# Optimization experiments

Hardware: AMD Instinct MI355X
Metric: run time of the kernel (lower is better)

Reference implementation:

```python
import jax, jax.numpy as jnp
import numpy as np

NUM_TAGS = 128
NUM_FEATURES = 500000
B, T, F = 64, 512, 8


def setup_inputs() -> dict:
    key = jax.random.key(0)
    ks = jax.random.split(key, 6)
    feats = jax.random.randint(ks[0], (B, T, F), 0, NUM_FEATURES)
    tags = jax.random.randint(ks[1], (B, T), 0, NUM_TAGS)
    # original init: uniform(-0.01, 0.01)
    state_weights = jax.random.uniform(ks[2], (NUM_TAGS, NUM_FEATURES), minval=-0.01, maxval=0.01, dtype=jnp.float32)
    transitions = jax.random.uniform(ks[3], (NUM_TAGS, NUM_TAGS), minval=-0.01, maxval=0.01, dtype=jnp.float32)
    start_transitions = jax.random.uniform(ks[4], (NUM_TAGS,), minval=-0.01, maxval=0.01, dtype=jnp.float32)
    end_transitions = jax.random.uniform(ks[5], (NUM_TAGS,), minval=-0.01, maxval=0.01, dtype=jnp.float32)
    return dict(feats=feats, tags=tags, state_weights=state_weights,
                transitions=transitions, start_transitions=start_transitions,
                end_transitions=end_transitions)


def reference(feats, tags, state_weights, transitions, start_transitions, end_transitions):
    """Batched CRF negative log-likelihood per sentence: logZ - gold_score. Returns [B]."""
    # emissions[b,t,k] = sum_f state_weights[k, feats[b,t,f]]  (emissions_for_sentence)
    emissions = jnp.take(state_weights, feats, axis=1).sum(-1)   # [K,B,T]
    emissions = jnp.moveaxis(emissions, 0, -1)                    # [B,T,K]

    # log_partition: forward algorithm over T via scan
    alpha0 = start_transitions[None, :] + emissions[:, 0]         # [B,K]

    def step(alpha, em_t):
        # scores[b,i,j] = alpha[b,i] + transitions[i,j]
        scores = alpha[:, :, None] + transitions[None, :, :]
        return jax.nn.logsumexp(scores, axis=1) + em_t, None

    em_rest = jnp.moveaxis(emissions[:, 1:], 1, 0)                # [T-1,B,K]
    alphaT, _ = jax.lax.scan(step, alpha0, em_rest)
    log_z = jax.nn.logsumexp(alphaT + end_transitions[None, :], axis=1)   # [B]

    # gold_score, vectorized over batch
    em_gold = jnp.take_along_axis(emissions, tags[..., None], axis=2)[..., 0].sum(axis=1)  # [B]
    trans_gold = transitions[tags[:, :-1], tags[:, 1:]].sum(axis=1)                        # [B]
    gold = start_transitions[tags[:, 0]] + end_transitions[tags[:, -1]] + em_gold + trans_gold

    return log_z - gold
```

## Files before the change

### kernel.cpp

```cpp
#include <hip/hip_runtime.h>

#define NUM_TAGS 128
#define NUM_FEATS 500000
#define BB 64
#define TT 512
#define FF 8

#define SWT_BYTES 256000000ull
#define EM_BYTES  16777216ull
#define NEED_FULL (SWT_BYTES + EM_BYTES)

typedef float f2 __attribute__((ext_vector_type(2)));

#define AP(j) ((((j) >> 5) * 36) + ((j) & 31))

__device__ __forceinline__ void barrier_lds() {
  asm volatile("s_waitcnt lgkmcnt(0)" ::: "memory");
  __builtin_amdgcn_s_barrier();
  __builtin_amdgcn_sched_barrier(0);
}

__device__ __forceinline__ float quad_sum_dpp(float r) {
  int t1 = __builtin_amdgcn_mov_dpp(__builtin_bit_cast(int, r), 0xB1, 0xF, 0xF, true);
  r += __builtin_bit_cast(float, t1);
  int t2 = __builtin_amdgcn_mov_dpp(__builtin_bit_cast(int, r), 0x4E, 0xF, 0xF, true);
  r += __builtin_bit_cast(float, t2);
  return r;
}

__global__ __launch_bounds__(256) void transpose_kernel(
    const float* __restrict__ sw, float* __restrict__ swT) {
  __shared__ float tile[32][129];
  const int f0 = blockIdx.x * 32;
  const int t = threadIdx.x;
  const int fi = t & 31, kb = t >> 5;
#pragma unroll
  for (int it = 0; it < 16; ++it) {
    int k = kb + it * 8;
    tile[fi][k] = sw[(size_t)k * NUM_FEATS + f0 + fi];
  }
  __syncthreads();
  const int k2 = t & 127, fo = t >> 7;
#pragma unroll
  for (int it = 0; it < 16; ++it) {
    int f2i = fo + it * 2;
    swT[(size_t)(f0 + f2i) * NUM_TAGS + k2] = tile[f2i][k2];
  }
}

__global__ __launch_bounds__(128) void gather_t_kernel(
    const int* __restrict__ feats, const float* __restrict__ swT,
    float* __restrict__ em_exp) {
  const int token = blockIdx.x;
  const int k = threadIdx.x;
  const int* f = feats + token * FF;
  float s = 0.f;
#pragma unroll
  for (int i = 0; i < FF; ++i) s += swT[(size_t)f[i] * NUM_TAGS + k];
  em_exp[(size_t)token * NUM_TAGS + k] = __expf(s);
}

__global__ __launch_bounds__(128) void gather_f_kernel(
    const int* __restrict__ feats, const float* __restrict__ sw,
    float* __restrict__ em_exp) {
  const int token = blockIdx.x;
  const int k = threadIdx.x;
  const int* f = feats + token * FF;
  const float* row = sw + (size_t)k * NUM_FEATS;
  float s = 0.f;
#pragma unroll
  for (int i = 0; i < FF; ++i) s += row[f[i]];
  em_exp[(size_t)token * NUM_TAGS + k] = __expf(s);
}

#define EINIT(I) (f2){__expf(trans[(32 * q + 2 * (I)) * NUM_TAGS + j]), \
                      __expf(trans[(32 * q + 2 * (I) + 1) * NUM_TAGS + j])}

#define STEP(EV, T, SRC, DST) do {                                          \
  float ev_ = (EV);                                                         \
  int tp_ = (T) + 4; if (tp_ > TT - 1) tp_ = TT - 1;                        \
  (EV) = embx[tp_ * NUM_TAGS + j];                    \
  const float4* a4_ = (const float4*)((SRC) + q * 36);                      \
  float4 A0 = a4_[0], A1 = a4_[1], A2 = a4_[2], A3 = a4_[3];                \
  float4 A4 = a4_[4], A5 = a4_[5], A6 = a4_[6], A7 = a4_[7];                \
  f2 ac0 = {0.f, 0.f}, ac1 = {0.f, 0.f};                                    \
  ac0 += (f2){A0.x, A0.y} * e00;  ac1 += (f2){A0.z, A0.w} * e01;            \
  ac0 += (f2){A1.x, A1.y} * e02;  ac1 += (f2){A1.z, A1.w} * e03;            \
  ac0 += (f2){A2.x, A2.y} * e04;  ac1 += (f2){A2.z, A2.w} * e05;            \
  ac0 += (f2){A3.x, A3.y} * e06;  ac1 += (f2){A3.z, A3.w} * e07;            \
  ac0 += (f2){A4.x, A4.y} * e08;  ac1 += (f2){A4.z, A4.w} * e09;            \
  ac0 += (f2){A5.x, A5.y} * e10;  ac1 += (f2){A5.z, A5.w} * e11;            \
  ac0 += (f2){A6.x, A6.y} * e12;  ac1 += (f2){A6.z, A6.w} * e13;            \
  ac0 += (f2){A7.x, A7.y} * e14;  ac1 += (f2){A7.z, A7.w} * e15;            \
  f2 s_ = ac0 + ac1;                                                        \
  float r_ = quad_sum_dpp(s_.x + s_.y);                                     \
  if (q == 0) (DST)[AP(j)] = r_ * ev_ * 0.0078125f;     \
  barrier_lds();                                                            \
} while (0)

__global__ __launch_bounds__(512, 1) void fwd_kernel(
    const float* __restrict__ em_exp, const int* __restrict__ tags,
    const float* __restrict__ trans, const float* __restrict__ startT,
    const float* __restrict__ endT, float* __restrict__ out) {
  const int b = blockIdx.x;
  const int tid = threadIdx.x;
  const int j = tid >> 2, q = tid & 3;

  __shared__ __align__(16) float alf[2][144];
  __shared__ float sred[16];

  f2 e00 = EINIT(0),  e01 = EINIT(1),  e02 = EINIT(2),  e03 = EINIT(3);
  f2 e04 = EINIT(4),  e05 = EINIT(5),  e06 = EINIT(6),  e07 = EINIT(7);
  f2 e08 = EINIT(8),  e09 = EINIT(9),  e10 = EINIT(10), e11 = EINIT(11);
  f2 e12 = EINIT(12), e13 = EINIT(13), e14 = EINIT(14), e15 = EINIT(15);

  const float* embx = em_exp + (size_t)b * TT * NUM_TAGS;

  if (q == 0) alf[0][AP(j)] = __expf(startT[j]) * embx[j];

  float evA = embx[1 * NUM_TAGS + j], evB = embx[2 * NUM_TAGS + j],
        evC = embx[3 * NUM_TAGS + j], evD = embx[4 * NUM_TAGS + j];
  __syncthreads();

  int cur = 0;
  for (int t = 1; t + 3 < TT; t += 4) {
    STEP(evA, t + 0, alf[cur], alf[cur ^ 1]); cur ^= 1;
    STEP(evB, t + 1, alf[cur], alf[cur ^ 1]); cur ^= 1;
    STEP(evC, t + 2, alf[cur], alf[cur ^ 1]); cur ^= 1;
    STEP(evD, t + 3, alf[cur], alf[cur ^ 1]); cur ^= 1;
  }
  STEP(evA, 509, alf[cur], alf[cur ^ 1]); cur ^= 1;
  STEP(evB, 510, alf[cur], alf[cur ^ 1]); cur ^= 1;
  STEP(evC, 511, alf[cur], alf[cur ^ 1]); cur ^= 1;

  if (tid < 128) {
    float val = alf[cur][AP(tid)] * __expf(endT[tid]);
#pragma unroll
    for (int off = 32; off > 0; off >>= 1) val += __shfl_down(val, off, 64);
    if ((tid & 63) == 0) sred[tid >> 6] = val;
  }

  const int* tb = tags + b * TT;
  const int t = tid;
  const int tg = tb[t];
  float g = __logf(embx[t * NUM_TAGS + tg]);
  if (t < TT - 1) g += trans[tg * NUM_TAGS + tb[t + 1]];
  if (t == 0) g += startT[tb[0]] + endT[tb[TT - 1]];
#pragma unroll
  for (int off = 32; off > 0; off >>= 1) g += __shfl_down(g, off, 64);
  if ((tid & 63) == 0) sred[8 + (tid >> 6)] = g;
  __syncthreads();

  if (tid == 0) {
    float logz = __logf(sred[0] + sred[1]) + 511.0f * 7.0f * 0.69314718055994531f;
    float gs = 0.f;
#pragma unroll
    for (int i = 0; i < 8; ++i) gs += sred[8 + i];
    out[b] = logz - gs;
  }
}

extern "C" void kernel_launch(void* const* d_in, const int* in_sizes, int n_in,
                              void* d_out, int out_size, void* d_ws, size_t ws_size,
                              hipStream_t stream) {
  const int* feats = (const int*)d_in[0];
  const int* tags = (const int*)d_in[1];
  const float* sw = (const float*)d_in[2];
  const float* trans = (const float*)d_in[3];
  const float* startT = (const float*)d_in[4];
  const float* endT = (const float*)d_in[5];
  float* out = (float*)d_out;

  if (ws_size >= NEED_FULL) {
    float* swT = (float*)d_ws;
    float* em_exp = (float*)((char*)d_ws + SWT_BYTES);
    transpose_kernel<<<NUM_FEATS / 32, 256, 0, stream>>>(sw, swT);
    gather_t_kernel<<<BB * TT, 128, 0, stream>>>(feats, swT, em_exp);
    fwd_kernel<<<BB, 512, 0, stream>>>(em_exp, tags, trans, startT, endT, out);
  } else {
    float* em_exp = (float*)d_ws;
    gather_f_kernel<<<BB * TT, 128, 0, stream>>>(feats, sw, em_exp);
    fwd_kernel<<<BB, 512, 0, stream>>>(em_exp, tags, trans, startT, endT, out);
  }
}
```

Baseline: 538.8 us.

## Replace transpose+gather with per-tag row gather split over feature halves

Drops the full 256MB transpose of state_weights. Instead, each block takes one tag row (optionally half of its feature range) and gathers the emissions for all tokens into a tag-major partial buffer, so each row's reads stay local and cacheable. The exp of emissions moves into the forward kernel, which now reads tag-major partials, sums the two halves and exponentiates per step, and the gold score uses raw emissions without a log. The risk is that only 128 or 256 blocks run the gather, and every block re-reads all token features, which may limit parallelism.

```diff
diff --git a/kernel.cpp b/kernel.cpp
--- a/kernel.cpp
+++ b/kernel.cpp
@@ -5,10 +5,7 @@
 #define BB 64
 #define TT 512
 #define FF 8
-
-#define SWT_BYTES 256000000ull
-#define EM_BYTES  16777216ull
-#define NEED_FULL (SWT_BYTES + EM_BYTES)
+#define NTOK (BB * TT)
 
 typedef float f2 __attribute__((ext_vector_type(2)));
 
@@ -28,58 +25,59 @@
   return r;
 }
 
-__global__ __launch_bounds__(256) void transpose_kernel(
-    const float* __restrict__ sw, float* __restrict__ swT) {
-  __shared__ float tile[32][129];
-  const int f0 = blockIdx.x * 32;
-  const int t = threadIdx.x;
-  const int fi = t & 31, kb = t >> 5;
-#pragma unroll
-  for (int it = 0; it < 16; ++it) {
-    int k = kb + it * 8;
-    tile[fi][k] = sw[(size_t)k * NUM_FEATS + f0 + fi];
+template <int NH>
+__global__ __launch_bounds__(512) void gather_k_kernel(
+    const int* __restrict__ feats, const float* __restrict__ sw,
+    float* __restrict__ emT) {
+  const int k = blockIdx.x & (NUM_TAGS - 1);
+  const int h = blockIdx.x >> 7;
+  const unsigned lo = h * (NUM_FEATS / NH);
+  const unsigned HF = NUM_FEATS / NH;
+  const float* __restrict__ row = sw + (size_t)k * NUM_FEATS;
+  float* __restrict__ outk = emT + (size_t)h * NUM_TAGS * NTOK + (size_t)k * NTOK;
+  const int tid = threadIdx.x;
+  for (int p = 0; p < NTOK / 1024; ++p) {
+    const int token = p * 1024 + tid * 2;
+    const int4* fp = (const int4*)(feats + (size_t)token * FF);
+    const int4 a = fp[0], b2 = fp[1], c = fp[2], d = fp[3];
+    float s0 = 0.f, s1 = 0.f;
+    if (NH == 1) {
+      s0 = ((row[a.x] + row[a.y]) + (row[a.z] + row[a.w])) +
+           ((row[b2.x] + row[b2.y]) + (row[b2.z] + row[b2.w]));
+      s1 = ((row[c.x] + row[c.y]) + (row[c.z] + row[c.w])) +
+           ((row[d.x] + row[d.y]) + (row[d.z] + row[d.w]));
+    } else {
+      if ((unsigned)(a.x - lo) < HF)  s0 += row[a.x];
+      if ((unsigned)(a.y - lo) < HF)  s0 += row[a.y];
+      if ((unsigned)(a.z - lo) < HF)  s0 += row[a.z];
+      if ((unsigned)(a.w - lo) < HF)  s0 += row[a.w];
+      if ((unsigned)(b2.x - lo) < HF) s0 += row[b2.x];
+      if ((unsigned)(b2.y - lo) < HF) s0 += row[b2.y];
+      if ((unsigned)(b2.z - lo) < HF) s0 += row[b2.z];
+      if ((unsigned)(b2.w - lo) < HF) s0 += row[b2.w];
+      if ((unsigned)(c.x - lo) < HF)  s1 += row[c.x];
+      if ((unsigned)(c.y - lo) < HF)  s1 += row[c.y];
+      if ((unsigned)(c.z - lo) < HF)  s1 += row[c.z];
+      if ((unsigned)(c.w - lo) < HF)  s1 += row[c.w];
+      if ((unsigned)(d.x - lo) < HF)  s1 += row[d.x];
+      if ((unsigned)(d.y - lo) < HF)  s1 += row[d.y];
+      if ((unsigned)(d.z - lo) < HF)  s1 += row[d.z];
+      if ((unsigned)(d.w - lo) < HF)  s1 += row[d.w];
+    }
+    outk[token] = s0;
+    outk[token + 1] = s1;
   }
-  __syncthreads();
-  const int k2 = t & 127, fo = t >> 7;
-#pragma unroll
-  for (int it = 0; it < 16; ++it) {
-    int f2i = fo + it * 2;
-    swT[(size_t)(f0 + f2i) * NUM_TAGS + k2] = tile[f2i][k2];
-  }
-}
-
-__global__ __launch_bounds__(128) void gather_t_kernel(
-    const int* __restrict__ feats, const float* __restrict__ swT,
-    float* __restrict__ em_exp) {
-  const int token = blockIdx.x;
-  const int k = threadIdx.x;
-  const int* f = feats + token * FF;
-  float s = 0.f;
-#pragma unroll
-  for (int i = 0; i < FF; ++i) s += swT[(size_t)f[i] * NUM_TAGS + k];
-  em_exp[(size_t)token * NUM_TAGS + k] = __expf(s);
-}
-
-__global__ __launch_bounds__(128) void gather_f_kernel(
-    const int* __restrict__ feats, const float* __restrict__ sw,
-    float* __restrict__ em_exp) {
-  const int token = blockIdx.x;
-  const int k = threadIdx.x;
-  const int* f = feats + token * FF;
-  const float* row = sw + (size_t)k * NUM_FEATS;
-  float s = 0.f;
-#pragma unroll
-  for (int i = 0; i < FF; ++i) s += row[f[i]];
-  em_exp[(size_t)token * NUM_TAGS + k] = __expf(s);
 }
 
 #define EINIT(I) (f2){__expf(trans[(32 * q + 2 * (I)) * NUM_TAGS + j]), \
                       __expf(trans[(32 * q + 2 * (I) + 1) * NUM_TAGS + j])}
 
 #define STEP(EV, T, SRC, DST) do {                                          \
-  float ev_ = (EV);                                                         \
+  f2 ep_ = (EV);                                                            \
   int tp_ = (T) + 4; if (tp_ > TT - 1) tp_ = TT - 1;                        \
-  (EV) = embx[tp_ * NUM_TAGS + j];                    \
+  (EV).x = jA[tp_];                                   \
+  (EV).y = TWO ? jB[tp_] : 0.f;                                             \
+  float ev_ = __expf(ep_.x + ep_.y);                                        \
   const float4* a4_ = (const float4*)((SRC) + q * 36);                      \
   float4 A0 = a4_[0], A1 = a4_[1], A2 = a4_[2], A3 = a4_[3];                \
   float4 A4 = a4_[4], A5 = a4_[5], A6 = a4_[6], A7 = a4_[7];                \
@@ -98,10 +96,12 @@
   barrier_lds();                                                            \
 } while (0)
 
+template <bool TWO>
 __global__ __launch_bounds__(512, 1) void fwd_kernel(
-    const float* __restrict__ em_exp, const int* __restrict__ tags,
-    const float* __restrict__ trans, const float* __restrict__ startT,
-    const float* __restrict__ endT, float* __restrict__ out) {
+    const float* __restrict__ pA, const float* __restrict__ pB,
+    const int* __restrict__ tags, const float* __restrict__ trans,
+    const float* __restrict__ startT, const float* __restrict__ endT,
+    float* __restrict__ out) {
   const int b = blockIdx.x;
   const int tid = threadIdx.x;
   const int j = tid >> 2, q = tid & 3;
@@ -114,12 +114,15 @@
   f2 e08 = EINIT(8),  e09 = EINIT(9),  e10 = EINIT(10), e11 = EINIT(11);
   f2 e12 = EINIT(12), e13 = EINIT(13), e14 = EINIT(14), e15 = EINIT(15);
 
-  const float* embx = em_exp + (size_t)b * TT * NUM_TAGS;
+  const float* __restrict__ jA = pA + (size_t)j * NTOK + b * TT;
+  const float* __restrict__ jB = pB + (size_t)j * NTOK + b * TT;
 
-  if (q == 0) alf[0][AP(j)] = __expf(startT[j]) * embx[j];
+  if (q == 0) alf[0][AP(j)] = __expf(startT[j] + jA[0] + (TWO ? jB[0] : 0.f));
 
-  float evA = embx[1 * NUM_TAGS + j], evB = embx[2 * NUM_TAGS + j],
-        evC = embx[3 * NUM_TAGS + j], evD = embx[4 * NUM_TAGS + j];
+  f2 evA = {jA[1], TWO ? jB[1] : 0.f};
+  f2 evB = {jA[2], TWO ? jB[2] : 0.f};
+  f2 evC = {jA[3], TWO ? jB[3] : 0.f};
+  f2 evD = {jA[4], TWO ? jB[4] : 0.f};
   __syncthreads();
 
   int cur = 0;
@@ -143,7 +146,8 @@
   const int* tb = tags + b * TT;
   const int t = tid;
   const int tg = tb[t];
-  float g = __logf(embx[t * NUM_TAGS + tg]);
+  float g = pA[(size_t)tg * NTOK + b * TT + t];
+  if (TWO) g += pB[(size_t)tg * NTOK + b * TT + t];
   if (t < TT - 1) g += trans[tg * NUM_TAGS + tb[t + 1]];
   if (t == 0) g += startT[tb[0]] + endT[tb[TT - 1]];
 #pragma unroll
@@ -171,15 +175,16 @@
   const float* endT = (const float*)d_in[5];
   float* out = (float*)d_out;
 
-  if (ws_size >= NEED_FULL) {
-    float* swT = (float*)d_ws;
-    float* em_exp = (float*)((char*)d_ws + SWT_BYTES);
-    transpose_kernel<<<NUM_FEATS / 32, 256, 0, stream>>>(sw, swT);
-    gather_t_kernel<<<BB * TT, 128, 0, stream>>>(feats, swT, em_exp);
-    fwd_kernel<<<BB, 512, 0, stream>>>(em_exp, tags, trans, startT, endT, out);
+  float* part = (float*)d_ws;
+  const size_t HALF_BYTES = (size_t)NUM_TAGS * NTOK * 4;
+
+  if (ws_size >= 2 * HALF_BYTES) {
+    gather_k_kernel<2><<<2 * NUM_TAGS, 512, 0, stream>>>(feats, sw, part);
+    fwd_kernel<true><<<BB, 512, 0, stream>>>(part, part + NUM_TAGS * NTOK,
+                                             tags, trans, startT, endT, out);
   } else {
-    float* em_exp = (float*)d_ws;
-    gather_f_kernel<<<BB * TT, 128, 0, stream>>>(feats, sw, em_exp);
-    fwd_kernel<<<BB, 512, 0, stream>>>(em_exp, tags, trans, startT, endT, out);
+    gather_k_kernel<1><<<NUM_TAGS, 512, 0, stream>>>(feats, sw, part);
+    fwd_kernel<false><<<BB, 512, 0, stream>>>(part, part,
+                                              tags, trans, startT, endT, out);
   }
 }
```

New measurement: 938.6 us. 74.2% more time.

## Process two batch sequences per forward-recursion block to interleave independent chains

Applied to the files above, without the earlier changes.

The forward kernel now handles two sentences per 512-thread block, advancing both alpha recursions in one step with one shared barrier. This is meant to hide LDS and barrier latency on the serial T-step chain by giving each step two independent dependency chains. The cost is that only 32 blocks run instead of 64, so fewer CUs are busy, and register pressure rises. The serial chain is latency-bound and 64 blocks already underfill the GPU, so halving the block count may cost little.

```diff
diff --git a/kernel.cpp b/kernel.cpp
--- a/kernel.cpp
+++ b/kernel.cpp
@@ -76,87 +76,129 @@
 #define EINIT(I) (f2){__expf(trans[(32 * q + 2 * (I)) * NUM_TAGS + j]), \
                       __expf(trans[(32 * q + 2 * (I) + 1) * NUM_TAGS + j])}
 
-#define STEP(EV, T, SRC, DST) do {                                          \
-  float ev_ = (EV);                                                         \
-  int tp_ = (T) + 4; if (tp_ > TT - 1) tp_ = TT - 1;                        \
-  (EV) = embx[tp_ * NUM_TAGS + j];                    \
-  const float4* a4_ = (const float4*)((SRC) + q * 36);                      \
-  float4 A0 = a4_[0], A1 = a4_[1], A2 = a4_[2], A3 = a4_[3];                \
-  float4 A4 = a4_[4], A5 = a4_[5], A6 = a4_[6], A7 = a4_[7];                \
-  f2 ac0 = {0.f, 0.f}, ac1 = {0.f, 0.f};                                    \
-  ac0 += (f2){A0.x, A0.y} * e00;  ac1 += (f2){A0.z, A0.w} * e01;            \
-  ac0 += (f2){A1.x, A1.y} * e02;  ac1 += (f2){A1.z, A1.w} * e03;            \
-  ac0 += (f2){A2.x, A2.y} * e04;  ac1 += (f2){A2.z, A2.w} * e05;            \
-  ac0 += (f2){A3.x, A3.y} * e06;  ac1 += (f2){A3.z, A3.w} * e07;            \
-  ac0 += (f2){A4.x, A4.y} * e08;  ac1 += (f2){A4.z, A4.w} * e09;            \
-  ac0 += (f2){A5.x, A5.y} * e10;  ac1 += (f2){A5.z, A5.w} * e11;            \
-  ac0 += (f2){A6.x, A6.y} * e12;  ac1 += (f2){A6.z, A6.w} * e13;            \
-  ac0 += (f2){A7.x, A7.y} * e14;  ac1 += (f2){A7.z, A7.w} * e15;            \
-  f2 s_ = ac0 + ac1;                                                        \
-  float r_ = quad_sum_dpp(s_.x + s_.y);                                     \
-  if (q == 0) (DST)[AP(j)] = r_ * ev_ * 0.0078125f;     \
-  barrier_lds();                                                            \
+#define STEP2(EVA, EVB, T, SA, DA, SB, DB) do {                              \
+  float eva_ = (EVA), evb_ = (EVB);                                          \
+  int tp_ = (T) + 4; if (tp_ > TT - 1) tp_ = TT - 1;                         \
+  (EVA) = embxA[tp_ * NUM_TAGS + j];                   \
+  (EVB) = embxB[tp_ * NUM_TAGS + j];                                         \
+  const float4* pa_ = (const float4*)((SA) + q * 36);                        \
+  const float4* pb_ = (const float4*)((SB) + q * 36);                        \
+  float4 A0 = pa_[0], A1 = pa_[1], A2 = pa_[2], A3 = pa_[3];                 \
+  float4 A4 = pa_[4], A5 = pa_[5], A6 = pa_[6], A7 = pa_[7];                 \
+  float4 B0 = pb_[0], B1 = pb_[1], B2 = pb_[2], B3 = pb_[3];                 \
+  float4 B4 = pb_[4], B5 = pb_[5], B6 = pb_[6], B7 = pb_[7];                 \
+  f2 aa0 = {0.f, 0.f}, aa1 = {0.f, 0.f};                                     \
+  f2 bb0 = {0.f, 0.f}, bb1 = {0.f, 0.f};                                     \
+  aa0 += (f2){A0.x, A0.y} * e00;  aa1 += (f2){A0.z, A0.w} * e01;             \
+  bb0 += (f2){B0.x, B0.y} * e00;  bb1 += (f2){B0.z, B0.w} * e01;             \
+  aa0 += (f2){A1.x, A1.y} * e02;  aa1 += (f2){A1.z, A1.w} * e03;             \
+  bb0 += (f2){B1.x, B1.y} * e02;  bb1 += (f2){B1.z, B1.w} * e03;             \
+  aa0 += (f2){A2.x, A2.y} * e04;  aa1 += (f2){A2.z, A2.w} * e05;             \
+  bb0 += (f2){B2.x, B2.y} * e04;  bb1 += (f2){B2.z, B2.w} * e05;             \
+  aa0 += (f2){A3.x, A3.y} * e06;  aa1 += (f2){A3.z, A3.w} * e07;             \
+  bb0 += (f2){B3.x, B3.y} * e06;  bb1 += (f2){B3.z, B3.w} * e07;             \
+  aa0 += (f2){A4.x, A4.y} * e08;  aa1 += (f2){A4.z, A4.w} * e09;             \
+  bb0 += (f2){B4.x, B4.y} * e08;  bb1 += (f2){B4.z, B4.w} * e09;             \
+  aa0 += (f2){A5.x, A5.y} * e10;  aa1 += (f2){A5.z, A5.w} * e11;             \
+  bb0 += (f2){B5.x, B5.y} * e10;  bb1 += (f2){B5.z, B5.w} * e11;             \
+  aa0 += (f2){A6.x, A6.y} * e12;  aa1 += (f2){A6.z, A6.w} * e13;             \
+  bb0 += (f2){B6.x, B6.y} * e12;  bb1 += (f2){B6.z, B6.w} * e13;             \
+  aa0 += (f2){A7.x, A7.y} * e14;  aa1 += (f2){A7.z, A7.w} * e15;             \
+  bb0 += (f2){B7.x, B7.y} * e14;  bb1 += (f2){B7.z, B7.w} * e15;             \
+  f2 sa_ = aa0 + aa1, sb_ = bb0 + bb1;                                       \
+  float ra_ = quad_sum_dpp(sa_.x + sa_.y);                                   \
+  float rb_ = quad_sum_dpp(sb_.x + sb_.y);                                   \
+  if (q == 0) {                                                              \
+    (DA)[AP(j)] = ra_ * eva_ * 0.0078125f;               \
+    (DB)[AP(j)] = rb_ * evb_ * 0.0078125f;                                   \
+  }                                                                          \
+  barrier_lds();                                                             \
 } while (0)
 
-__global__ __launch_bounds__(512, 1) void fwd_kernel(
+__global__ __launch_bounds__(512, 1) void fwd2_kernel(
     const float* __restrict__ em_exp, const int* __restrict__ tags,
     const float* __restrict__ trans, const float* __restrict__ startT,
     const float* __restrict__ endT, float* __restrict__ out) {
-  const int b = blockIdx.x;
+  const int b0 = 2 * blockIdx.x, b1 = 2 * blockIdx.x + 1;
   const int tid = threadIdx.x;
   const int j = tid >> 2, q = tid & 3;
 
-  __shared__ __align__(16) float alf[2][144];
-  __shared__ float sred[16];
+  __shared__ __align__(16) float alfA[2][144];
+  __shared__ __align__(16) float alfB[2][144];
+  __shared__ float sredA[16], sredB[16];
 
   f2 e00 = EINIT(0),  e01 = EINIT(1),  e02 = EINIT(2),  e03 = EINIT(3);
   f2 e04 = EINIT(4),  e05 = EINIT(5),  e06 = EINIT(6),  e07 = EINIT(7);
   f2 e08 = EINIT(8),  e09 = EINIT(9),  e10 = EINIT(10), e11 = EINIT(11);
   f2 e12 = EINIT(12), e13 = EINIT(13), e14 = EINIT(14), e15 = EINIT(15);
 
-  const float* embx = em_exp + (size_t)b * TT * NUM_TAGS;
-
-  if (q == 0) alf[0][AP(j)] = __expf(startT[j]) * embx[j];
-
-  float evA = embx[1 * NUM_TAGS + j], evB = embx[2 * NUM_TAGS + j],
-        evC = embx[3 * NUM_TAGS + j], evD = embx[4 * NUM_TAGS + j];
+  const float* embxA = em_exp + (size_t)b0 * TT * NUM_TAGS;
+  const float* embxB = em_exp + (size_t)b1 * TT * NUM_TAGS;
+
+  if (q == 0) {
+    alfA[0][AP(j)] = __expf(startT[j]) * embxA[j];
+    alfB[0][AP(j)] = __expf(startT[j]) * embxB[j];
+  }
+
+  float evA0 = embxA[1 * NUM_TAGS + j], evB0 = embxA[2 * NUM_TAGS + j],
+        evC0 = embxA[3 * NUM_TAGS + j], evD0 = embxA[4 * NUM_TAGS + j];
+  float evA1 = embxB[1 * NUM_TAGS + j], evB1 = embxB[2 * NUM_TAGS + j],
+        evC1 = embxB[3 * NUM_TAGS + j], evD1 = embxB[4 * NUM_TAGS + j];
   __syncthreads();
 
   int cur = 0;
   for (int t = 1; t + 3 < TT; t += 4) {
-    STEP(evA, t + 0, alf[cur], alf[cur ^ 1]); cur ^= 1;
-    STEP(evB, t + 1, alf[cur], alf[cur ^ 1]); cur ^= 1;
-    STEP(evC, t + 2, alf[cur], alf[cur ^ 1]); cur ^= 1;
-    STEP(evD, t + 3, alf[cur], alf[cur ^ 1]); cur ^= 1;
-  }
-  STEP(evA, 509, alf[cur], alf[cur ^ 1]); cur ^= 1;
-  STEP(evB, 510, alf[cur], alf[cur ^ 1]); cur ^= 1;
-  STEP(evC, 511, alf[cur], alf[cur ^ 1]); cur ^= 1;
+    STEP2(evA0, evA1, t + 0, alfA[cur], alfA[cur ^ 1], alfB[cur], alfB[cur ^ 1]); cur ^= 1;
+    STEP2(evB0, evB1, t + 1, alfA[cur], alfA[cur ^ 1], alfB[cur], alfB[cur ^ 1]); cur ^= 1;
+    STEP2(evC0, evC1, t + 2, alfA[cur], alfA[cur ^ 1], alfB[cur], alfB[cur ^ 1]); cur ^= 1;
+    STEP2(evD0, evD1, t + 3, alfA[cur], alfA[cur ^ 1], alfB[cur], alfB[cur ^ 1]); cur ^= 1;
+  }
+  STEP2(evA0, evA1, 509, alfA[cur], alfA[cur ^ 1], alfB[cur], alfB[cur ^ 1]); cur ^= 1;
+  STEP2(evB0, evB1, 510, alfA[cur], alfA[cur ^ 1], alfB[cur], alfB[cur ^ 1]); cur ^= 1;
+  STEP2(evC0, evC1, 511, alfA[cur], alfA[cur ^ 1], alfB[cur], alfB[cur ^ 1]); cur ^= 1;
 
   if (tid < 128) {
-    float val = alf[cur][AP(tid)] * __expf(endT[tid]);
+    float val = alfA[cur][AP(tid)] * __expf(endT[tid]);
 #pragma unroll
     for (int off = 32; off > 0; off >>= 1) val += __shfl_down(val, off, 64);
-    if ((tid & 63) == 0) sred[tid >> 6] = val;
-  }
-
-  const int* tb = tags + b * TT;
-  const int t = tid;
-  const int tg = tb[t];
-  float g = __logf(embx[t * NUM_TAGS + tg]);
-  if (t < TT - 1) g += trans[tg * NUM_TAGS + tb[t + 1]];
-  if (t == 0) g += startT[tb[0]] + endT[tb[TT - 1]];
-#pragma unroll
-  for (int off = 32; off > 0; off >>= 1) g += __shfl_down(g, off, 64);
-  if ((tid & 63) == 0) sred[8 + (tid >> 6)] = g;
+    if ((tid & 63) == 0) sredA[tid >> 6] = val;
+  } else if (tid < 256) {
+    const int j2 = tid - 128;
+    float val = alfB[cur][AP(j2)] * __expf(endT[j2]);
+#pragma unroll
+    for (int off = 32; off > 0; off >>= 1) val += __shfl_down(val, off, 64);
+    if ((tid & 63) == 0) sredB[(tid >> 6) & 1] = val;
+  }
+
+  {
+    const int* tb = tags + b0 * TT;
+    const int tg = tb[tid];
+    float g = __logf(embxA[tid * NUM_TAGS + tg]);
+    if (tid < TT - 1) g += trans[tg * NUM_TAGS + tb[tid + 1]];
+    if (tid == 0) g += startT[tb[0]] + endT[tb[TT - 1]];
+#pragma unroll
+    for (int off = 32; off > 0; off >>= 1) g += __shfl_down(g, off, 64);
+    if ((tid & 63) == 0) sredA[8 + (tid >> 6)] = g;
+  }
+  {
+    const int* tb = tags + b1 * TT;
+    const int tg = tb[tid];
+    float g = __logf(embxB[tid * NUM_TAGS + tg]);
+    if (tid < TT - 1) g += trans[tg * NUM_TAGS + tb[tid + 1]];
+    if (tid == 0) g += startT[tb[0]] + endT[tb[TT - 1]];
+#pragma unroll
+    for (int off = 32; off > 0; off >>= 1) g += __shfl_down(g, off, 64);
+    if ((tid & 63) == 0) sredB[8 + (tid >> 6)] = g;
+  }
   __syncthreads();
 
   if (tid == 0) {
-    float logz = __logf(sred[0] + sred[1]) + 511.0f * 7.0f * 0.69314718055994531f;
-    float gs = 0.f;
-#pragma unroll
-    for (int i = 0; i < 8; ++i) gs += sred[8 + i];
-    out[b] = logz - gs;
+    const float KLOG = 511.0f * 7.0f * 0.69314718055994531f;
+    float gsA = 0.f, gsB = 0.f;
+#pragma unroll
+    for (int i = 0; i < 8; ++i) { gsA += sredA[8 + i]; gsB += sredB[8 + i]; }
+    out[b0] = __logf(sredA[0] + sredA[1]) + KLOG - gsA;
+    out[b1] = __logf(sredB[0] + sredB[1]) + KLOG - gsB;
   }
 }
 
@@ -176,10 +218,10 @@
     float* em_exp = (float*)((char*)d_ws + SWT_BYTES);
     transpose_kernel<<<NUM_FEATS / 32, 256, 0, stream>>>(sw, swT);
     gather_t_kernel<<<BB * TT, 128, 0, stream>>>(feats, swT, em_exp);
-    fwd_kernel<<<BB, 512, 0, stream>>>(em_exp, tags, trans, startT, endT, out);
+    fwd2_kernel<<<BB / 2, 512, 0, stream>>>(em_exp, tags, trans, startT, endT, out);
   } else {
     float* em_exp = (float*)d_ws;
     gather_f_kernel<<<BB * TT, 128, 0, stream>>>(feats, sw, em_exp);
-    fwd_kernel<<<BB, 512, 0, stream>>>(em_exp, tags, trans, startT, endT, out);
-  }
-}
+    fwd2_kernel<<<BB / 2, 512, 0, stream>>>(em_exp, tags, trans, startT, endT, out);
+  }
+}
```

After: 620.5 us. 15.2% more time.

## Halve forward-kernel block size, computing two tags per thread

Applied to the files above, without the earlier changes.

The forward-recursion kernel drops from 512 to 256 threads per block. Each thread now holds two sets of exp(transition) registers and computes alpha for tags j and j+64 in every step. The gold-score pass loops over two timesteps per thread so all 512 positions are still covered. The aim is to make the per-step LDS barrier cheaper by syncing 4 waves instead of 8, at the cost of doubled ALU work and register pressure per thread on the serial critical path.

```diff
diff --git a/kernel.cpp b/kernel.cpp
--- a/kernel.cpp
+++ b/kernel.cpp
@@ -75,30 +75,46 @@
 
 #define EINIT(I) (f2){__expf(trans[(32 * q + 2 * (I)) * NUM_TAGS + j]), \
                       __expf(trans[(32 * q + 2 * (I) + 1) * NUM_TAGS + j])}
+#define FINIT(I) (f2){__expf(trans[(32 * q + 2 * (I)) * NUM_TAGS + j + 64]), \
+                      __expf(trans[(32 * q + 2 * (I) + 1) * NUM_TAGS + j + 64])}
 
 #define STEP(EV, T, SRC, DST) do {                                          \
-  float ev_ = (EV);                                                         \
+  f2 ev_ = (EV);                                                            \
   int tp_ = (T) + 4; if (tp_ > TT - 1) tp_ = TT - 1;                        \
-  (EV) = embx[tp_ * NUM_TAGS + j];                    \
+  (EV).x = embx[tp_ * NUM_TAGS + j];                  \
+  (EV).y = embx[tp_ * NUM_TAGS + j + 64];                                   \
   const float4* a4_ = (const float4*)((SRC) + q * 36);                      \
   float4 A0 = a4_[0], A1 = a4_[1], A2 = a4_[2], A3 = a4_[3];                \
   float4 A4 = a4_[4], A5 = a4_[5], A6 = a4_[6], A7 = a4_[7];                \
   f2 ac0 = {0.f, 0.f}, ac1 = {0.f, 0.f};                                    \
+  f2 bc0 = {0.f, 0.f}, bc1 = {0.f, 0.f};                                    \
   ac0 += (f2){A0.x, A0.y} * e00;  ac1 += (f2){A0.z, A0.w} * e01;            \
+  bc0 += (f2){A0.x, A0.y} * f00;  bc1 += (f2){A0.z, A0.w} * f01;            \
   ac0 += (f2){A1.x, A1.y} * e02;  ac1 += (f2){A1.z, A1.w} * e03;            \
+  bc0 += (f2){A1.x, A1.y} * f02;  bc1 += (f2){A1.z, A1.w} * f03;            \
   ac0 += (f2){A2.x, A2.y} * e04;  ac1 += (f2){A2.z, A2.w} * e05;            \
+  bc0 += (f2){A2.x, A2.y} * f04;  bc1 += (f2){A2.z, A2.w} * f05;            \
   ac0 += (f2){A3.x, A3.y} * e06;  ac1 += (f2){A3.z, A3.w} * e07;            \
+  bc0 += (f2){A3.x, A3.y} * f06;  bc1 += (f2){A3.z, A3.w} * f07;            \
   ac0 += (f2){A4.x, A4.y} * e08;  ac1 += (f2){A4.z, A4.w} * e09;            \
+  bc0 += (f2){A4.x, A4.y} * f08;  bc1 += (f2){A4.z, A4.w} * f09;            \
   ac0 += (f2){A5.x, A5.y} * e10;  ac1 += (f2){A5.z, A5.w} * e11;            \
+  bc0 += (f2){A5.x, A5.y} * f10;  bc1 += (f2){A5.z, A5.w} * f11;            \
   ac0 += (f2){A6.x, A6.y} * e12;  ac1 += (f2){A6.z, A6.w} * e13;            \
+  bc0 += (f2){A6.x, A6.y} * f12;  bc1 += (f2){A6.z, A6.w} * f13;            \
   ac0 += (f2){A7.x, A7.y} * e14;  ac1 += (f2){A7.z, A7.w} * e15;            \
-  f2 s_ = ac0 + ac1;                                                        \
-  float r_ = quad_sum_dpp(s_.x + s_.y);                                     \
-  if (q == 0) (DST)[AP(j)] = r_ * ev_ * 0.0078125f;     \
+  bc0 += (f2){A7.x, A7.y} * f14;  bc1 += (f2){A7.z, A7.w} * f15;            \
+  f2 sa_ = ac0 + ac1, sb_ = bc0 + bc1;                                      \
+  float ra_ = quad_sum_dpp(sa_.x + sa_.y);                                  \
+  float rb_ = quad_sum_dpp(sb_.x + sb_.y);                                  \
+  if (q == 0) {                                                             \
+    (DST)[AP(j)] = ra_ * ev_.x * 0.0078125f;            \
+    (DST)[AP(j + 64)] = rb_ * ev_.y * 0.0078125f;                           \
+  }                                                                         \
   barrier_lds();                                                            \
 } while (0)
 
-__global__ __launch_bounds__(512, 1) void fwd_kernel(
+__global__ __launch_bounds__(256, 1) void fwd_kernel(
     const float* __restrict__ em_exp, const int* __restrict__ tags,
     const float* __restrict__ trans, const float* __restrict__ startT,
     const float* __restrict__ endT, float* __restrict__ out) {
@@ -113,13 +129,22 @@
   f2 e04 = EINIT(4),  e05 = EINIT(5),  e06 = EINIT(6),  e07 = EINIT(7);
   f2 e08 = EINIT(8),  e09 = EINIT(9),  e10 = EINIT(10), e11 = EINIT(11);
   f2 e12 = EINIT(12), e13 = EINIT(13), e14 = EINIT(14), e15 = EINIT(15);
+  f2 f00 = FINIT(0),  f01 = FINIT(1),  f02 = FINIT(2),  f03 = FINIT(3);
+  f2 f04 = FINIT(4),  f05 = FINIT(5),  f06 = FINIT(6),  f07 = FINIT(7);
+  f2 f08 = FINIT(8),  f09 = FINIT(9),  f10 = FINIT(10), f11 = FINIT(11);
+  f2 f12 = FINIT(12), f13 = FINIT(13), f14 = FINIT(14), f15 = FINIT(15);
 
   const float* embx = em_exp + (size_t)b * TT * NUM_TAGS;
 
-  if (q == 0) alf[0][AP(j)] = __expf(startT[j]) * embx[j];
-
-  float evA = embx[1 * NUM_TAGS + j], evB = embx[2 * NUM_TAGS + j],
-        evC = embx[3 * NUM_TAGS + j], evD = embx[4 * NUM_TAGS + j];
+  if (q == 0) {
+    alf[0][AP(j)] = __expf(startT[j]) * embx[j];
+    alf[0][AP(j + 64)] = __expf(startT[j + 64]) * embx[j + 64];
+  }
+
+  f2 evA = {embx[1 * NUM_TAGS + j], embx[1 * NUM_TAGS + j + 64]};
+  f2 evB = {embx[2 * NUM_TAGS + j], embx[2 * NUM_TAGS + j + 64]};
+  f2 evC = {embx[3 * NUM_TAGS + j], embx[3 * NUM_TAGS + j + 64]};
+  f2 evD = {embx[4 * NUM_TAGS + j], embx[4 * NUM_TAGS + j + 64]};
   __syncthreads();
 
   int cur = 0;
@@ -141,11 +166,15 @@
   }
 
   const int* tb = tags + b * TT;
-  const int t = tid;
-  const int tg = tb[t];
-  float g = __logf(embx[t * NUM_TAGS + tg]);
-  if (t < TT - 1) g += trans[tg * NUM_TAGS + tb[t + 1]];
-  if (t == 0) g += startT[tb[0]] + endT[tb[TT - 1]];
+  float g = 0.f;
+#pragma unroll
+  for (int p = 0; p < 2; ++p) {
+    const int t = tid + 256 * p;
+    const int tg = tb[t];
+    g += __logf(embx[t * NUM_TAGS + tg]);
+    if (t < TT - 1) g += trans[tg * NUM_TAGS + tb[t + 1]];
+  }
+  if (tid == 0) g += startT[tb[0]] + endT[tb[TT - 1]];
 #pragma unroll
   for (int off = 32; off > 0; off >>= 1) g += __shfl_down(g, off, 64);
   if ((tid & 63) == 0) sred[8 + (tid >> 6)] = g;
@@ -155,7 +184,7 @@
     float logz = __logf(sred[0] + sred[1]) + 511.0f * 7.0f * 0.69314718055994531f;
     float gs = 0.f;
 #pragma unroll
-    for (int i = 0; i < 8; ++i) gs += sred[8 + i];
+    for (int i = 0; i < 4; ++i) gs += sred[8 + i];
     out[b] = logz - gs;
   }
 }
@@ -176,10 +205,10 @@
     float* em_exp = (float*)((char*)d_ws + SWT_BYTES);
     transpose_kernel<<<NUM_FEATS / 32, 256, 0, stream>>>(sw, swT);
     gather_t_kernel<<<BB * TT, 128, 0, stream>>>(feats, swT, em_exp);
-    fwd_kernel<<<BB, 512, 0, stream>>>(em_exp, tags, trans, startT, endT, out);
+    fwd_kernel<<<BB, 256, 0, stream>>>(em_exp, tags, trans, startT, endT, out);
   } else {
     float* em_exp = (float*)d_ws;
     gather_f_kernel<<<BB * TT, 128, 0, stream>>>(feats, sw, em_exp);
-    fwd_kernel<<<BB, 512, 0, stream>>>(em_exp, tags, trans, startT, endT, out);
-  }
-}
+    fwd_kernel<<<BB, 256, 0, stream>>>(em_exp, tags, trans, startT, endT, out);
+  }
+}
```

Result: no change. 545.8 us (+1.3%).
